# Kernel tuning notes

Hardware: AMD Instinct MI355X
Metric: run time of the kernel (lower is better)

Reference implementation:

```python
import jax, jax.numpy as jnp
import numpy as np

B, S, C = 2, 2048, 1536
HQ, HKV, DQK, DV = 8, 1, 128, 192
G = HQ // HKV
MAX_POS = 8192
CLIP = 5.0
EPS = 1e-5


def rms_bn(x, scale):
    # RMSBatchNorm: per-channel RMS over batch+seq dims, learnable scale (assumed, class not in source)
    ms = jnp.mean(jnp.square(x), axis=(0, 1), keepdims=True)
    return x * jax.lax.rsqrt(ms + EPS) * scale


def layer_norm(x, w, b):
    mu = jnp.mean(x, axis=-1, keepdims=True)
    var = jnp.mean(jnp.square(x - mu), axis=-1, keepdims=True)
    return (x - mu) * jax.lax.rsqrt(var + EPS) * w + b


def apply_rope(x, max_position):
    # x: [B, S, *, Ch] with even Ch; custom AlphaGenome frequency schedule
    s = x.shape[1]
    ch = x.shape[-1]
    nf = ch // 2
    dt = x.dtype
    lin = jnp.arange(nf, dtype=dt)
    if nf > max_position:
        geom = jnp.ones((nf,), dtype=dt)
    else:
        geom = jnp.exp(jnp.linspace(jnp.log(jnp.asarray(1.0, dt)), jnp.log(jnp.asarray(max_position - nf + 1.0, dt)), nf))
    inv_freq = 1.0 / (lin + geom)
    pos = jnp.arange(s, dtype=dt)
    theta = pos[:, None] * inv_freq  # [S, nf]
    extra = x.ndim - 3
    theta = theta.reshape((1, s) + (1,) * extra + (nf,))
    theta = jnp.repeat(theta, 2, axis=-1)  # interleaved freqs -> [.., Ch]
    x_rot = jnp.stack([-x[..., 1::2], x[..., ::2]], axis=-1).reshape(x.shape)
    return x * jnp.cos(theta) + x_rot * jnp.sin(theta)


def setup_inputs() -> dict:
    key = jax.random.key(0)
    ks = jax.random.split(key, 8)
    sq = lambda fan_in: 1.0 / np.sqrt(fan_in)
    return {
        "x": jax.random.normal(ks[0], (B, S, C), jnp.float32),
        "bn1_scale": jnp.ones((C,), jnp.float32),
        "q_w": jax.random.normal(ks[1], (HQ * DQK, C), jnp.float32) * sq(C),
        "k_w": jax.random.normal(ks[2], (HKV * DQK, C), jnp.float32) * sq(C),
        "v_w": jax.random.normal(ks[3], (HKV * DV, C), jnp.float32) * sq(C),
        "qn_w": jnp.ones((DQK,), jnp.float32), "qn_b": jnp.zeros((DQK,), jnp.float32),
        "kn_w": jnp.ones((DQK,), jnp.float32), "kn_b": jnp.zeros((DQK,), jnp.float32),
        "vn_w": jnp.ones((DV,), jnp.float32), "vn_b": jnp.zeros((DV,), jnp.float32),
        "bn2_scale": jnp.ones((C,), jnp.float32),
        "out_w": jax.random.normal(ks[4], (C, HQ * DV), jnp.float32) * sq(HQ * DV),
        "out_b": jnp.zeros((C,), jnp.float32),
    }


def reference(x, bn1_scale, q_w, k_w, v_w, qn_w, qn_b, kn_w, kn_b, vn_w, vn_b, bn2_scale, out_w, out_b):
    xb = rms_bn(x, bn1_scale)
    q = (xb @ q_w.T).reshape(B, S, G, HKV, DQK)
    k = (xb @ k_w.T).reshape(B, S, HKV, DQK)
    v = (xb @ v_w.T).reshape(B, S, HKV, DV)
    q = layer_norm(q, qn_w, qn_b)
    k = layer_norm(k, kn_w, kn_b)
    v = layer_norm(v, vn_w, vn_b)
    q = apply_rope(q, MAX_POS)
    k = apply_rope(k, MAX_POS)
    logits = jnp.einsum("bsghc,bthc->bghst", q, k) / np.sqrt(DQK)
    logits = jnp.tanh(logits / CLIP) * CLIP
    attn = jax.nn.softmax(logits, axis=-1)
    y = jnp.einsum("bghst,bthc->bsghc", attn, v)
    y = y.reshape(B, S, HQ * DV)
    y = y @ out_w.T + out_b
    y = rms_bn(y, bn2_scale)
    return y
```

## Files before the change

### kernel.cpp

```cpp
#include <hip/hip_runtime.h>
#include <hip/hip_bf16.h>
#include <math.h>

#define Bb 2
#define Ss 2048
#define Cc 1536
#define HQ 8
#define DQK 128
#define DV 192
#define ROWS (Bb*Ss)
#define NQKV 1408
#define EPSf 1e-5f
#define CLIPf 5.0f

typedef short short8 __attribute__((ext_vector_type(8)));
typedef float f32x4 __attribute__((ext_vector_type(4)));
typedef unsigned short ushort;
typedef ushort us4 __attribute__((ext_vector_type(4)));

__device__ __forceinline__ float wave_sum(float v) {
#pragma unroll
    for (int off = 32; off >= 1; off >>= 1) v += __shfl_xor(v, off);
    return v;
}

__device__ __forceinline__ ushort bf16_bits(float f) {
    __hip_bfloat16 hb = __float2bfloat16(f);
    return *reinterpret_cast<ushort*>(&hb);
}

__device__ __forceinline__ void gld16(const void* g, void* l) {
    __builtin_amdgcn_global_load_lds(
        (const __attribute__((address_space(1))) void*)g,
        (__attribute__((address_space(3))) void*)l, 16, 0, 0);
}

__global__ void sq_reduce(const float* __restrict__ x, float* __restrict__ ms, int ncols) {
    int ch = blockIdx.x * blockDim.x + threadIdx.x;
    int r0 = blockIdx.y * 128;
    float acc = 0.f;
    for (int r = r0; r < r0 + 128; ++r) {
        float v = x[(size_t)r * ncols + ch];
        acc += v * v;
    }
    atomicAdd(&ms[ch], acc);
}

template <int BF16>
__global__ void rms_apply_v(const float* __restrict__ x, const float* __restrict__ ms,
                            const float* __restrict__ scale, void* __restrict__ outp,
                            int ncols4, size_t total4) {
    for (size_t i = (size_t)blockIdx.x * blockDim.x + threadIdx.x; i < total4;
         i += (size_t)gridDim.x * blockDim.x) {
        int c4 = (int)(i % ncols4);
        float4 v = ((const float4*)x)[i];
        float4 m4 = ((const float4*)ms)[c4];
        float4 s4 = ((const float4*)scale)[c4];
        float o0 = v.x * rsqrtf(m4.x * (1.0f / ROWS) + EPSf) * s4.x;
        float o1 = v.y * rsqrtf(m4.y * (1.0f / ROWS) + EPSf) * s4.y;
        float o2 = v.z * rsqrtf(m4.z * (1.0f / ROWS) + EPSf) * s4.z;
        float o3 = v.w * rsqrtf(m4.w * (1.0f / ROWS) + EPSf) * s4.w;
        if (BF16) {
            us4 o = {bf16_bits(o0), bf16_bits(o1), bf16_bits(o2), bf16_bits(o3)};
            ((us4*)outp)[i] = o;
        } else {
            float4 o = {o0, o1, o2, o3};
            ((float4*)outp)[i] = o;
        }
    }
}

__global__ void cvt_bf16(const float* __restrict__ in, ushort* __restrict__ out, int n4) {
    int i = blockIdx.x * blockDim.x + threadIdx.x;
    if (i >= n4) return;
    float4 v = ((const float4*)in)[i];
    us4 o = {bf16_bits(v.x), bf16_bits(v.y), bf16_bits(v.z), bf16_bits(v.w)};
    ((us4*)out)[i] = o;
}

__global__ __launch_bounds__(256) void gemm_bf16(const ushort* __restrict__ A,
                                                 const ushort* __restrict__ W,
                                                 const float* __restrict__ bias,
                                                 float* __restrict__ Cout,
                                                 int N, int K, int hasBias) {
    __shared__ ushort AS[4096];
    __shared__ ushort WS[4096];
    int tid = threadIdx.x;
    int w = tid >> 6, lane = tid & 63;
    int gl = lane >> 4, li = lane & 15;
    int wr = w >> 1, wc = w & 1;
    int m0 = blockIdx.y * 128, n0 = blockIdx.x * 128;

    int r = tid & 127, gg = tid >> 7;
    const ushort* pA = A + (size_t)(m0 + r) * K + gg * 8;
    const ushort* pW = W + (size_t)(n0 + r) * K + gg * 8;
    ushort* lA0 = &AS[w * 512];
    ushort* lA1 = &AS[2048 + w * 512];
    ushort* lW0 = &WS[w * 512];
    ushort* lW1 = &WS[2048 + w * 512];

    const ushort* fA = &AS[(gl * 128 + wr * 64 + li) * 8];
    const ushort* fW = &WS[(gl * 128 + wc * 64 + li) * 8];

    f32x4 acc[4][4];
#pragma unroll
    for (int m = 0; m < 4; ++m)
#pragma unroll
        for (int n = 0; n < 4; ++n) acc[m][n] = (f32x4){0.f, 0.f, 0.f, 0.f};

    for (int kk = 0; kk < K; kk += 32) {
        __syncthreads();
        gld16(pA + kk, lA0);
        gld16(pA + kk + 16, lA1);
        gld16(pW + kk, lW0);
        gld16(pW + kk + 16, lW1);
        __syncthreads();
        short8 a[4], b[4];
#pragma unroll
        for (int m = 0; m < 4; ++m) a[m] = *(const short8*)(fA + m * 128);
#pragma unroll
        for (int n = 0; n < 4; ++n) b[n] = *(const short8*)(fW + n * 128);
#pragma unroll
        for (int m = 0; m < 4; ++m)
#pragma unroll
            for (int n = 0; n < 4; ++n)
                acc[m][n] = __builtin_amdgcn_mfma_f32_16x16x32_bf16(a[m], b[n], acc[m][n], 0, 0, 0);
    }

#pragma unroll
    for (int m = 0; m < 4; ++m) {
        int row = m0 + wr * 64 + m * 16 + gl * 4;
#pragma unroll
        for (int n = 0; n < 4; ++n) {
            int col = n0 + wc * 64 + n * 16 + li;
            float bv = hasBias ? bias[col] : 0.0f;
#pragma unroll
            for (int rr = 0; rr < 4; ++rr)
                Cout[(size_t)(row + rr) * N + col] = acc[m][n][rr] + bv;
        }
    }
}

template <int D, int ROPE>
__global__ void ln_rope_w(const float* __restrict__ in, ushort* __restrict__ outb,
                          const float* __restrict__ w, const float* __restrict__ b,
                          int gdiv, int rstride, int coff, int nrows) {
    int wid = blockIdx.x * (blockDim.x >> 6) + (threadIdx.x >> 6);
    if (wid >= nrows) return;
    int lane = threadIdx.x & 63;
    const float* src = in + (size_t)(wid / gdiv) * rstride + (size_t)(wid % gdiv) * D + coff;

    if (D == 128) {
        float2 e = *(const float2*)&src[2 * lane];
        float mu = wave_sum(e.x + e.y) * (1.0f / D);
        float d0 = e.x - mu, d1 = e.y - mu;
        float var = wave_sum(d0 * d0 + d1 * d1) * (1.0f / D);
        float rs = rsqrtf(var + EPSf);
        float n0 = d0 * rs * w[2 * lane] + b[2 * lane];
        float n1 = d1 * rs * w[2 * lane + 1] + b[2 * lane + 1];
        float r0 = n0, r1 = n1;
        if (ROPE) {
            int s = (wid / gdiv) % Ss;
            float geom = expf((float)lane * (logf(8129.0f) / 63.0f));
            float invf = 1.0f / ((float)lane + geom);
            float th = (float)s * invf;
            float ct = cosf(th), st = sinf(th);
            r0 = n0 * ct - n1 * st;
            r1 = n1 * ct + n0 * st;
        }
        ushort2 o = {bf16_bits(r0), bf16_bits(r1)};
        *(ushort2*)&outb[(size_t)wid * D + 2 * lane] = o;
    } else {
        float e0 = src[lane], e1 = src[lane + 64], e2 = src[lane + 128];
        float mu = wave_sum(e0 + e1 + e2) * (1.0f / D);
        float d0 = e0 - mu, d1 = e1 - mu, d2 = e2 - mu;
        float var = wave_sum(d0 * d0 + d1 * d1 + d2 * d2) * (1.0f / D);
        float rs = rsqrtf(var + EPSf);
        outb[(size_t)wid * D + lane]       = bf16_bits(d0 * rs * w[lane] + b[lane]);
        outb[(size_t)wid * D + lane + 64]  = bf16_bits(d1 * rs * w[lane + 64] + b[lane + 64]);
        outb[(size_t)wid * D + lane + 128] = bf16_bits(d2 * rs * w[lane + 128] + b[lane + 128]);
    }
}

__global__ __launch_bounds__(256) void transpose_v(const ushort* __restrict__ vbh,
                                                   ushort* __restrict__ vT) {
    __shared__ ushort tb[64][72];
    int t0 = blockIdx.x * 64, d0 = blockIdx.y * 64, b = blockIdx.z;
    int tid = threadIdx.x;
#pragma unroll
    for (int i = 0; i < 2; ++i) {
        int ci = tid + i * 256;
        int t = ci >> 3, dc = ci & 7;
        short8 v = *(const short8*)&vbh[((size_t)(b * Ss + t0 + t)) * DV + d0 + dc * 8];
        *(short8*)&tb[t][dc * 8] = v;
    }
    __syncthreads();
#pragma unroll
    for (int i = 0; i < 2; ++i) {
        int ci = tid + i * 256;
        int d = ci >> 3, tc = ci & 7;
        short8 v;
#pragma unroll
        for (int j = 0; j < 8; ++j) v[j] = (short)tb[tc * 8 + j][d];
        *(short8*)&vT[((size_t)(b * DV + d0 + d)) * Ss + t0 + tc * 8] = v;
    }
}

__global__ __launch_bounds__(256, 2) void attn_mfma(const ushort* __restrict__ qbh,
                                                    const ushort* __restrict__ kbh,
                                                    const ushort* __restrict__ vT,
                                                    ushort* __restrict__ yab) {
    __shared__ ushort Klds[64 * 128];
    __shared__ ushort VTlds[192 * 64];
    __shared__ ushort Plds[4 * 16 * 64];
    int tid = threadIdx.x;
    int b = blockIdx.z, gq = blockIdx.y;
    int q0 = blockIdx.x * 64;
    int w = tid >> 6, lane = tid & 63;
    int g = lane >> 4, li = lane & 15;
    int mask = (li & 7) << 4;

    short8 qf[4];
    {
        int qrow = q0 + w * 16 + li;
        const ushort* qptr = qbh + ((size_t)(b * Ss + qrow) * HQ + gq) * DQK + g * 8;
#pragma unroll
        for (int c = 0; c < 4; ++c) qf[c] = *(const short8*)(qptr + c * 32);
    }

    f32x4 pv[12];
#pragma unroll
    for (int n = 0; n < 12; ++n) pv[n] = (f32x4){0.f, 0.f, 0.f, 0.f};
    float lacc[4] = {0.f, 0.f, 0.f, 0.f};

    const float scl = 0.088388347648318447f;

    for (int kt = 0; kt < Ss / 64; ++kt) {
        int t0 = kt * 64;
#pragma unroll
        for (int i = 0; i < 4; ++i) {
            int ci = tid + i * 256;
            int row = ci >> 4, cb = ci & 15;
            short8 v = *(const short8*)&kbh[(size_t)(b * Ss + t0 + row) * DQK + cb * 8];
            *(short8*)((char*)Klds + ((row * 256 + cb * 16) ^ ((row & 7) << 4))) = v;
        }
#pragma unroll
        for (int i = 0; i < 6; ++i) {
            int ci = tid + i * 256;
            int row = ci >> 3, cb = ci & 7;
            short8 v = *(const short8*)&vT[((size_t)(b * DV + row)) * Ss + t0 + cb * 8];
            *(short8*)((char*)VTlds + ((row * 128 + cb * 16) ^ ((row & 7) << 4))) = v;
        }
        __syncthreads();

        f32x4 s[4];
#pragma unroll
        for (int n = 0; n < 4; ++n) s[n] = (f32x4){0.f, 0.f, 0.f, 0.f};
#pragma unroll
        for (int c = 0; c < 4; ++c) {
#pragma unroll
            for (int n = 0; n < 4; ++n) {
                short8 kf = *(const short8*)((char*)Klds +
                            ((li * 256 + g * 16 + n * 4096 + c * 64) ^ mask));
                s[n] = __builtin_amdgcn_mfma_f32_16x16x32_bf16(qf[c], kf, s[n], 0, 0, 0);
            }
        }

        float rsum[4] = {0.f, 0.f, 0.f, 0.f};
#pragma unroll
        for (int n = 0; n < 4; ++n) {
#pragma unroll
            for (int rr = 0; rr < 4; ++rr) {
                float z = s[n][rr] * scl;
                float u = __expf(0.4f * z);
                float p = __expf(5.0f - 10.0f * __builtin_amdgcn_rcpf(u + 1.0f));
                rsum[rr] += p;
                int row = g * 4 + rr;
                *(ushort*)((char*)Plds + w * 2048 +
                           ((row * 128 + n * 32 + li * 2) ^ ((row & 7) << 4))) = bf16_bits(p);
            }
        }
#pragma unroll
        for (int rr = 0; rr < 4; ++rr) {
            float v = rsum[rr];
            v += __shfl_xor(v, 1); v += __shfl_xor(v, 2);
            v += __shfl_xor(v, 4); v += __shfl_xor(v, 8);
            lacc[rr] += v;
        }

#pragma unroll
        for (int c2 = 0; c2 < 2; ++c2) {
            short8 pa = *(const short8*)((char*)Plds + w * 2048 +
                        ((li * 128 + c2 * 64 + g * 16) ^ mask));
#pragma unroll
            for (int n = 0; n < 12; ++n) {
                short8 vf = *(const short8*)((char*)VTlds +
                            ((n * 2048 + li * 128 + c2 * 64 + g * 16) ^ mask));
                pv[n] = __builtin_amdgcn_mfma_f32_16x16x32_bf16(pa, vf, pv[n], 0, 0, 0);
            }
        }
        __syncthreads();
    }

    float invl[4];
#pragma unroll
    for (int rr = 0; rr < 4; ++rr) invl[rr] = 1.0f / lacc[rr];
#pragma unroll
    for (int n = 0; n < 12; ++n) {
#pragma unroll
        for (int rr = 0; rr < 4; ++rr) {
            int qr = q0 + w * 16 + g * 4 + rr;
            yab[((size_t)(b * Ss + qr) * HQ + gq) * DV + n * 16 + li] =
                bf16_bits(pv[n][rr] * invl[rr]);
        }
    }
}

extern "C" void kernel_launch(void* const* d_in, const int* in_sizes, int n_in,
                              void* d_out, int out_size, void* d_ws, size_t ws_size,
                              hipStream_t stream) {
    const float* x         = (const float*)d_in[0];
    const float* bn1_scale = (const float*)d_in[1];
    const float* q_w       = (const float*)d_in[2];
    const float* k_w       = (const float*)d_in[3];
    const float* v_w       = (const float*)d_in[4];
    const float* qn_w      = (const float*)d_in[5];
    const float* qn_b      = (const float*)d_in[6];
    const float* kn_w      = (const float*)d_in[7];
    const float* kn_b      = (const float*)d_in[8];
    const float* vn_w      = (const float*)d_in[9];
    const float* vn_b      = (const float*)d_in[10];
    const float* bn2_scale = (const float*)d_in[11];
    const float* out_w     = (const float*)d_in[12];
    const float* out_b     = (const float*)d_in[13];
    float* out = (float*)d_out;

    char* wsb = (char*)d_ws;
    float* ms1 = (float*)wsb;
    float* ms2 = ms1 + Cc;
    char* base = wsb + 16384;
    ushort* xbh   = (ushort*)base;
    ushort* qkvwh = xbh + (size_t)ROWS * Cc;
    float*  qkvb  = (float*)(qkvwh + (size_t)NQKV * Cc);
    ushort* owh   = (ushort*)(qkvb + (size_t)ROWS * NQKV);
    ushort* qbh   = owh + (size_t)Cc * Cc;
    ushort* kbh   = qbh + (size_t)ROWS * HQ * DQK;
    ushort* vbh   = kbh + (size_t)ROWS * DQK;
    ushort* vTb   = vbh + (size_t)ROWS * DV;
    ushort* yab   = vTb + (size_t)Bb * DV * Ss;
    float*  proj  = (float*)base;

    hipMemsetAsync(ms1, 0, 2 * Cc * sizeof(float), stream);

    sq_reduce<<<dim3(Cc / 256, ROWS / 128), 256, 0, stream>>>(x, ms1, Cc);
    rms_apply_v<1><<<2048, 256, 0, stream>>>(x, ms1, bn1_scale, xbh, Cc / 4,
                                             (size_t)ROWS * Cc / 4);

    cvt_bf16<<<(HQ * DQK * Cc / 4 + 255) / 256, 256, 0, stream>>>(q_w, qkvwh, HQ * DQK * Cc / 4);
    cvt_bf16<<<(DQK * Cc / 4 + 255) / 256, 256, 0, stream>>>(k_w, qkvwh + (size_t)1024 * Cc, DQK * Cc / 4);
    cvt_bf16<<<(DV * Cc / 4 + 255) / 256, 256, 0, stream>>>(v_w, qkvwh + (size_t)1152 * Cc, DV * Cc / 4);
    cvt_bf16<<<(Cc * Cc / 4 + 255) / 256, 256, 0, stream>>>(out_w, owh, Cc * Cc / 4);

    gemm_bf16<<<dim3(NQKV / 128, ROWS / 128), 256, 0, stream>>>(
        xbh, qkvwh, nullptr, qkvb, NQKV, Cc, 0);

    ln_rope_w<DQK, 1><<<ROWS * HQ / 4, 256, 0, stream>>>(qkvb, qbh, qn_w, qn_b, HQ, NQKV, 0, ROWS * HQ);
    ln_rope_w<DQK, 1><<<ROWS / 4, 256, 0, stream>>>(qkvb, kbh, kn_w, kn_b, 1, NQKV, 1024, ROWS);
    ln_rope_w<DV, 0><<<ROWS / 4, 256, 0, stream>>>(qkvb, vbh, vn_w, vn_b, 1, NQKV, 1152, ROWS);

    transpose_v<<<dim3(Ss / 64, DV / 64, Bb), 256, 0, stream>>>(vbh, vTb);

    attn_mfma<<<dim3(Ss / 64, HQ, Bb), 256, 0, stream>>>(qbh, kbh, vTb, yab);

    gemm_bf16<<<dim3(Cc / 128, ROWS / 128), 256, 0, stream>>>(
        yab, owh, out_b, proj, Cc, Cc, 1);

    sq_reduce<<<dim3(Cc / 256, ROWS / 128), 256, 0, stream>>>(proj, ms2, Cc);
    rms_apply_v<0><<<2048, 256, 0, stream>>>(proj, ms2, bn2_scale, out, Cc / 4,
                                             (size_t)ROWS * Cc / 4);
}
```

Baseline: 370.3 us.

## Merge weight converts and LN kernels, emit bf16 QKV, prefetch K/V in attention

Several unrelated changes land together. The four weight-cast launches become one cvt_all kernel, and the three layernorm/rope launches become one ln_all kernel. The QKV GEMM now writes bf16 instead of fp32, which halves the intermediate traffic at some precision cost before layernorm. The attention kernel register-prefetches the next K/V tile while computing the current one, and its launch bounds move to 3 blocks per SM, which adds register pressure and risks spills.

```diff
diff --git a/kernel.cpp b/kernel.cpp
--- a/kernel.cpp
+++ b/kernel.cpp
@@ -27,6 +27,11 @@
 __device__ __forceinline__ ushort bf16_bits(float f) {
     __hip_bfloat16 hb = __float2bfloat16(f);
     return *reinterpret_cast<ushort*>(&hb);
+}
+
+__device__ __forceinline__ float bfu(ushort u) {
+    unsigned v = (unsigned)u << 16;
+    return *reinterpret_cast<float*>(&v);
 }
 
 __device__ __forceinline__ void gld16(const void* g, void* l) {
@@ -70,18 +75,29 @@
     }
 }
 
-__global__ void cvt_bf16(const float* __restrict__ in, ushort* __restrict__ out, int n4) {
-    int i = blockIdx.x * blockDim.x + threadIdx.x;
-    if (i >= n4) return;
-    float4 v = ((const float4*)in)[i];
+__global__ void cvt_all(const float* __restrict__ q_w, const float* __restrict__ k_w,
+                        const float* __restrict__ v_w, const float* __restrict__ ow,
+                        ushort* __restrict__ qkvwh, ushort* __restrict__ owh) {
+    const int QN = 1024 * Cc / 4, KN = 128 * Cc / 4, VN = 192 * Cc / 4, ON = Cc * Cc / 4;
+    int i = blockIdx.x * 256 + threadIdx.x;
+    const float* src;
+    us4* dst;
+    int off;
+    if (i < QN)                  { src = q_w; dst = (us4*)qkvwh;                         off = i; }
+    else if (i < QN + KN)        { src = k_w; dst = (us4*)(qkvwh + (size_t)1024 * Cc);   off = i - QN; }
+    else if (i < QN + KN + VN)   { src = v_w; dst = (us4*)(qkvwh + (size_t)1152 * Cc);   off = i - QN - KN; }
+    else if (i < QN + KN + VN + ON) { src = ow; dst = (us4*)owh;                         off = i - QN - KN - VN; }
+    else return;
+    float4 v = ((const float4*)src)[off];
     us4 o = {bf16_bits(v.x), bf16_bits(v.y), bf16_bits(v.z), bf16_bits(v.w)};
-    ((us4*)out)[i] = o;
-}
-
+    dst[off] = o;
+}
+
+template <int OUTBF16>
 __global__ __launch_bounds__(256) void gemm_bf16(const ushort* __restrict__ A,
                                                  const ushort* __restrict__ W,
                                                  const float* __restrict__ bias,
-                                                 float* __restrict__ Cout,
+                                                 void* __restrict__ Cout,
                                                  int N, int K, int hasBias) {
     __shared__ ushort AS[4096];
     __shared__ ushort WS[4096];
@@ -135,50 +151,73 @@
             int col = n0 + wc * 64 + n * 16 + li;
             float bv = hasBias ? bias[col] : 0.0f;
 #pragma unroll
-            for (int rr = 0; rr < 4; ++rr)
-                Cout[(size_t)(row + rr) * N + col] = acc[m][n][rr] + bv;
-        }
-    }
-}
-
-template <int D, int ROPE>
-__global__ void ln_rope_w(const float* __restrict__ in, ushort* __restrict__ outb,
-                          const float* __restrict__ w, const float* __restrict__ b,
-                          int gdiv, int rstride, int coff, int nrows) {
-    int wid = blockIdx.x * (blockDim.x >> 6) + (threadIdx.x >> 6);
-    if (wid >= nrows) return;
+            for (int rr = 0; rr < 4; ++rr) {
+                float o = acc[m][n][rr] + bv;
+                if (OUTBF16)
+                    ((ushort*)Cout)[(size_t)(row + rr) * N + col] = bf16_bits(o);
+                else
+                    ((float*)Cout)[(size_t)(row + rr) * N + col] = o;
+            }
+        }
+    }
+}
+
+__global__ void ln_all(const ushort* __restrict__ qkv,
+                       ushort* __restrict__ qbh, ushort* __restrict__ kbh,
+                       ushort* __restrict__ vbh,
+                       const float* __restrict__ qn_w, const float* __restrict__ qn_b,
+                       const float* __restrict__ kn_w, const float* __restrict__ kn_b,
+                       const float* __restrict__ vn_w, const float* __restrict__ vn_b) {
+    int wid = blockIdx.x * 4 + (threadIdx.x >> 6);
     int lane = threadIdx.x & 63;
-    const float* src = in + (size_t)(wid / gdiv) * rstride + (size_t)(wid % gdiv) * D + coff;
-
-    if (D == 128) {
-        float2 e = *(const float2*)&src[2 * lane];
-        float mu = wave_sum(e.x + e.y) * (1.0f / D);
-        float d0 = e.x - mu, d1 = e.y - mu;
-        float var = wave_sum(d0 * d0 + d1 * d1) * (1.0f / D);
+
+    if (wid < ROWS * HQ + ROWS) {
+        const ushort* src;
+        ushort* dst;
+        const float* w;
+        const float* b;
+        int s;
+        if (wid < ROWS * HQ) {
+            int row = wid >> 3, h = wid & 7;
+            src = qkv + (size_t)row * NQKV + h * DQK;
+            dst = qbh + (size_t)wid * DQK;
+            w = qn_w; b = qn_b;
+            s = row % Ss;
+        } else {
+            int idx = wid - ROWS * HQ;
+            src = qkv + (size_t)idx * NQKV + 1024;
+            dst = kbh + (size_t)idx * DQK;
+            w = kn_w; b = kn_b;
+            s = idx % Ss;
+        }
+        ushort2 e2 = *(const ushort2*)&src[2 * lane];
+        float e0 = bfu(e2.x), e1 = bfu(e2.y);
+        float mu = wave_sum(e0 + e1) * (1.0f / DQK);
+        float d0 = e0 - mu, d1 = e1 - mu;
+        float var = wave_sum(d0 * d0 + d1 * d1) * (1.0f / DQK);
         float rs = rsqrtf(var + EPSf);
         float n0 = d0 * rs * w[2 * lane] + b[2 * lane];
         float n1 = d1 * rs * w[2 * lane + 1] + b[2 * lane + 1];
-        float r0 = n0, r1 = n1;
-        if (ROPE) {
-            int s = (wid / gdiv) % Ss;
-            float geom = expf((float)lane * (logf(8129.0f) / 63.0f));
-            float invf = 1.0f / ((float)lane + geom);
-            float th = (float)s * invf;
-            float ct = cosf(th), st = sinf(th);
-            r0 = n0 * ct - n1 * st;
-            r1 = n1 * ct + n0 * st;
-        }
+        float geom = expf((float)lane * (logf(8129.0f) / 63.0f));
+        float invf = 1.0f / ((float)lane + geom);
+        float th = (float)s * invf;
+        float ct = cosf(th), st = sinf(th);
+        float r0 = n0 * ct - n1 * st;
+        float r1 = n1 * ct + n0 * st;
         ushort2 o = {bf16_bits(r0), bf16_bits(r1)};
-        *(ushort2*)&outb[(size_t)wid * D + 2 * lane] = o;
+        *(ushort2*)&dst[2 * lane] = o;
     } else {
-        float e0 = src[lane], e1 = src[lane + 64], e2 = src[lane + 128];
-        float mu = wave_sum(e0 + e1 + e2) * (1.0f / D);
+        int idx = wid - ROWS * HQ - ROWS;
+        const ushort* src = qkv + (size_t)idx * NQKV + 1152;
+        ushort* dst = vbh + (size_t)idx * DV;
+        float e0 = bfu(src[lane]), e1 = bfu(src[lane + 64]), e2 = bfu(src[lane + 128]);
+        float mu = wave_sum(e0 + e1 + e2) * (1.0f / DV);
         float d0 = e0 - mu, d1 = e1 - mu, d2 = e2 - mu;
-        float var = wave_sum(d0 * d0 + d1 * d1 + d2 * d2) * (1.0f / D);
+        float var = wave_sum(d0 * d0 + d1 * d1 + d2 * d2) * (1.0f / DV);
         float rs = rsqrtf(var + EPSf);
-        outb[(size_t)wid * D + lane]       = bf16_bits(d0 * rs * w[lane] + b[lane]);
-        outb[(size_t)wid * D + lane + 64]  = bf16_bits(d1 * rs * w[lane + 64] + b[lane + 64]);
-        outb[(size_t)wid * D + lane + 128] = bf16_bits(d2 * rs * w[lane + 128] + b[lane + 128]);
+        dst[lane]       = bf16_bits(d0 * rs * vn_w[lane] + vn_b[lane]);
+        dst[lane + 64]  = bf16_bits(d1 * rs * vn_w[lane + 64] + vn_b[lane + 64]);
+        dst[lane + 128] = bf16_bits(d2 * rs * vn_w[lane + 128] + vn_b[lane + 128]);
     }
 }
 
@@ -206,7 +245,7 @@
     }
 }
 
-__global__ __launch_bounds__(256, 2) void attn_mfma(const ushort* __restrict__ qbh,
+__global__ __launch_bounds__(256, 3) void attn_mfma(const ushort* __restrict__ qbh,
                                                     const ushort* __restrict__ kbh,
                                                     const ushort* __restrict__ vT,
                                                     ushort* __restrict__ yab) {
@@ -228,6 +267,19 @@
         for (int c = 0; c < 4; ++c) qf[c] = *(const short8*)(qptr + c * 32);
     }
 
+    int krow0 = tid >> 4, kcb = tid & 15;
+    int vrow0 = tid >> 3, vcb = tid & 7;
+    const ushort* kbase = kbh + (size_t)b * Ss * DQK;
+    const ushort* vbase = vT + (size_t)b * DV * Ss;
+
+    short8 kreg[4], vreg[6];
+#pragma unroll
+    for (int i = 0; i < 4; ++i)
+        kreg[i] = *(const short8*)&kbase[(size_t)(krow0 + i * 16) * DQK + kcb * 8];
+#pragma unroll
+    for (int i = 0; i < 6; ++i)
+        vreg[i] = *(const short8*)&vbase[(size_t)(vrow0 + i * 32) * Ss + vcb * 8];
+
     f32x4 pv[12];
 #pragma unroll
     for (int n = 0; n < 12; ++n) pv[n] = (f32x4){0.f, 0.f, 0.f, 0.f};
@@ -236,22 +288,27 @@
     const float scl = 0.088388347648318447f;
 
     for (int kt = 0; kt < Ss / 64; ++kt) {
-        int t0 = kt * 64;
 #pragma unroll
         for (int i = 0; i < 4; ++i) {
-            int ci = tid + i * 256;
-            int row = ci >> 4, cb = ci & 15;
-            short8 v = *(const short8*)&kbh[(size_t)(b * Ss + t0 + row) * DQK + cb * 8];
-            *(short8*)((char*)Klds + ((row * 256 + cb * 16) ^ ((row & 7) << 4))) = v;
+            int row = krow0 + i * 16;
+            *(short8*)((char*)Klds + ((row * 256 + kcb * 16) ^ ((row & 7) << 4))) = kreg[i];
         }
 #pragma unroll
         for (int i = 0; i < 6; ++i) {
-            int ci = tid + i * 256;
-            int row = ci >> 3, cb = ci & 7;
-            short8 v = *(const short8*)&vT[((size_t)(b * DV + row)) * Ss + t0 + cb * 8];
-            *(short8*)((char*)VTlds + ((row * 128 + cb * 16) ^ ((row & 7) << 4))) = v;
+            int row = vrow0 + i * 32;
+            *(short8*)((char*)VTlds + ((row * 128 + vcb * 16) ^ ((row & 7) << 4))) = vreg[i];
         }
         __syncthreads();
+
+        if (kt + 1 < Ss / 64) {
+            int t1 = (kt + 1) * 64;
+#pragma unroll
+            for (int i = 0; i < 4; ++i)
+                kreg[i] = *(const short8*)&kbase[(size_t)(t1 + krow0 + i * 16) * DQK + kcb * 8];
+#pragma unroll
+            for (int i = 0; i < 6; ++i)
+                vreg[i] = *(const short8*)&vbase[(size_t)(vrow0 + i * 32) * Ss + t1 + vcb * 8];
+        }
 
         f32x4 s[4];
 #pragma unroll
@@ -341,8 +398,8 @@
     char* base = wsb + 16384;
     ushort* xbh   = (ushort*)base;
     ushort* qkvwh = xbh + (size_t)ROWS * Cc;
-    float*  qkvb  = (float*)(qkvwh + (size_t)NQKV * Cc);
-    ushort* owh   = (ushort*)(qkvb + (size_t)ROWS * NQKV);
+    ushort* qkvbh = qkvwh + (size_t)NQKV * Cc;
+    ushort* owh   = qkvbh + (size_t)ROWS * NQKV;
     ushort* qbh   = owh + (size_t)Cc * Cc;
     ushort* kbh   = qbh + (size_t)ROWS * HQ * DQK;
     ushort* vbh   = kbh + (size_t)ROWS * DQK;
@@ -356,23 +413,22 @@
     rms_apply_v<1><<<2048, 256, 0, stream>>>(x, ms1, bn1_scale, xbh, Cc / 4,
                                              (size_t)ROWS * Cc / 4);
 
-    cvt_bf16<<<(HQ * DQK * Cc / 4 + 255) / 256, 256, 0, stream>>>(q_w, qkvwh, HQ * DQK * Cc / 4);
-    cvt_bf16<<<(DQK * Cc / 4 + 255) / 256, 256, 0, stream>>>(k_w, qkvwh + (size_t)1024 * Cc, DQK * Cc / 4);
-    cvt_bf16<<<(DV * Cc / 4 + 255) / 256, 256, 0, stream>>>(v_w, qkvwh + (size_t)1152 * Cc, DV * Cc / 4);
-    cvt_bf16<<<(Cc * Cc / 4 + 255) / 256, 256, 0, stream>>>(out_w, owh, Cc * Cc / 4);
-
-    gemm_bf16<<<dim3(NQKV / 128, ROWS / 128), 256, 0, stream>>>(
-        xbh, qkvwh, nullptr, qkvb, NQKV, Cc, 0);
-
-    ln_rope_w<DQK, 1><<<ROWS * HQ / 4, 256, 0, stream>>>(qkvb, qbh, qn_w, qn_b, HQ, NQKV, 0, ROWS * HQ);
-    ln_rope_w<DQK, 1><<<ROWS / 4, 256, 0, stream>>>(qkvb, kbh, kn_w, kn_b, 1, NQKV, 1024, ROWS);
-    ln_rope_w<DV, 0><<<ROWS / 4, 256, 0, stream>>>(qkvb, vbh, vn_w, vn_b, 1, NQKV, 1152, ROWS);
+    {
+        int total4 = (1024 * Cc + 128 * Cc + 192 * Cc + Cc * Cc) / 4;
+        cvt_all<<<(total4 + 255) / 256, 256, 0, stream>>>(q_w, k_w, v_w, out_w, qkvwh, owh);
+    }
+
+    gemm_bf16<1><<<dim3(NQKV / 128, ROWS / 128), 256, 0, stream>>>(
+        xbh, qkvwh, nullptr, qkvbh, NQKV, Cc, 0);
+
+    ln_all<<<(ROWS * HQ + ROWS + ROWS) / 4, 256, 0, stream>>>(
+        qkvbh, qbh, kbh, vbh, qn_w, qn_b, kn_w, kn_b, vn_w, vn_b);
 
     transpose_v<<<dim3(Ss / 64, DV / 64, Bb), 256, 0, stream>>>(vbh, vTb);
 
     attn_mfma<<<dim3(Ss / 64, HQ, Bb), 256, 0, stream>>>(qbh, kbh, vTb, yab);
 
-    gemm_bf16<<<dim3(Cc / 128, ROWS / 128), 256, 0, stream>>>(
+    gemm_bf16<0><<<dim3(Cc / 128, ROWS / 128), 256, 0, stream>>>(
         yab, owh, out_b, proj, Cc, Cc, 1);
 
     sq_reduce<<<dim3(Cc / 256, ROWS / 128), 256, 0, stream>>>(proj, ms2, Cc);
```

Result: slower. 456.5 us (+23.3%).
